# Optimization experiments

Measured on AMD Instinct MI355X. Metric: run time of the kernel, lower is better.

Reference implementation:

```python
import jax, jax.numpy as jnp
import numpy as np

D = 512       # d_model
H = 8         # n_heads
HD = D // H   # head_dim = 64
BS = 64       # block_size
B = 1
S = 8192
NB = S // BS  # 128 blocks
THRESH = 0.3


def setup_inputs() -> dict:
    key = jax.random.key(0)
    ks = jax.random.split(key, 6)
    sc = 0.02
    return {
        "x": jax.random.normal(ks[0], (B, S, D), jnp.float32),
        "w_qkv": (jax.random.normal(ks[1], (D, 3 * D)) * sc).astype(jnp.float32),
        "b_qkv": jnp.zeros((3 * D,), jnp.float32),
        "w_out": (jax.random.normal(ks[2], (D, D)) * sc).astype(jnp.float32),
        "b_out": jnp.zeros((D,), jnp.float32),
        "w_r1": (jax.random.normal(ks[3], (D, 128)) * sc).astype(jnp.float32),
        "b_r1": jnp.zeros((128,), jnp.float32),
        "w_r2": (jax.random.normal(ks[4], (128, 1)) * sc).astype(jnp.float32),
        "b_r2": jnp.full((1,), 0.5, jnp.float32),  # sigmoid(~0.5)>0.3 -> non-degenerate mask
    }


def reference(x, w_qkv, b_qkv, w_out, b_out, w_r1, b_r1, w_r2, b_r2):
    Bx, Sx, Dx = x.shape
    qkv = (x @ w_qkv + b_qkv).reshape(Bx, Sx, 3, H, HD)
    q = jnp.transpose(qkv[:, :, 0], (0, 2, 1, 3))  # [B,H,S,HD]
    k = jnp.transpose(qkv[:, :, 1], (0, 2, 1, 3))
    v = jnp.transpose(qkv[:, :, 2], (0, 2, 1, 3))

    # --- router: per-block importance from mean-pooled q block (d_model features) ---
    qb = q.reshape(Bx, H, NB, BS, HD)
    rep = jnp.transpose(qb.mean(axis=3), (0, 2, 1, 3)).reshape(Bx, NB, Dx)  # [B,NB,D]
    imp = jax.nn.sigmoid(jax.nn.relu(rep @ w_r1 + b_r1) @ w_r2 + b_r2)[..., 0]  # [B,NB]
    keep = (imp.mean(axis=0) >= THRESH).astype(x.dtype)  # [NB], shared across batch (torch uses batch-mean)

    kb = k.reshape(Bx, H, NB, BS, HD)
    vb = v.reshape(Bx, H, NB, BS, HD)
    tri = jnp.triu(jnp.ones((BS, BS), bool), 1)  # strict upper triangle within diagonal block
    jidx = jnp.arange(NB)
    scale = 1.0 / np.sqrt(HD)

    def step(carry, i):
        q_i = jax.lax.dynamic_slice_in_dim(q, i * BS, BS, axis=2)        # [B,H,BSq,HD]
        s = jnp.einsum('bhqd,bhjkd->bhqjk', q_i, kb) * scale             # [B,H,BSq,NB,BSk]
        causal = (jidx == i)[None, :, None] & tri[:, None, :]            # [BSq,NB,BSk]
        s = jnp.where(causal[None, None], -jnp.inf, s)
        p = jax.nn.softmax(s, axis=-1)                                   # softmax PER key-block (as in torch loop)
        wj = keep * keep[i]                                              # block pair gate [NB]
        o = jnp.einsum('bhqjk,j,bhjkd->bhqd', p, wj, vb)                 # sum of gated per-block contributions
        return carry, o

    _, outs = jax.lax.scan(step, None, jnp.arange(NB))                   # [NB,B,H,BSq,HD]
    attn = jnp.transpose(outs, (1, 2, 0, 3, 4)).reshape(Bx, H, Sx, HD)
    attn = jnp.transpose(attn, (0, 2, 1, 3)).reshape(Bx, Sx, Dx)
    return attn @ w_out + b_out
```

## Files before the change

### kernel.cpp

```cpp
#include <hip/hip_runtime.h>

typedef unsigned short u16;
typedef unsigned int u32;
typedef __attribute__((ext_vector_type(8))) short short8;
typedef __attribute__((ext_vector_type(4))) short short4v;
typedef __attribute__((ext_vector_type(4))) float f32x4;
typedef __attribute__((ext_vector_type(4))) float float4v;
typedef __attribute__((ext_vector_type(2))) u32 u32x2;
typedef __attribute__((ext_vector_type(4))) u32 u32x4;

#define S_LEN 8192
#define NHEAD 8
#define NBLK  128
#define SCALE_C 0.18033688011112042f

__device__ __forceinline__ u16 f2b(float f) {
    union { float f; unsigned u; } v; v.f = f;
    unsigned r = v.u + 0x7FFFu + ((v.u >> 16) & 1u);
    return (u16)(r >> 16);
}
__device__ __forceinline__ float b2f(u16 b) {
    union { float f; unsigned u; } v; v.u = ((unsigned)b) << 16; return v.f;
}
__device__ __forceinline__ u32 cvt_pk_bf16(float lo, float hi) {
    u32 r;
    asm("v_cvt_pk_bf16_f32 %0, %1, %2" : "=v"(r) : "v"(lo), "v"(hi));
    return r;
}
__device__ __forceinline__ void pl16swap(u32& a, u32& b) {
    u32x2 r = __builtin_amdgcn_permlane16_swap(a, b, false, false);
    a = r[0]; b = r[1];
}
__device__ __forceinline__ void pl32swap(u32& a, u32& b) {
    u32x2 r = __builtin_amdgcn_permlane32_swap(a, b, false, false);
    a = r[0]; b = r[1];
}
__device__ __forceinline__ int swz(int row, int colByte) {
    return row * 128 + (colByte ^ ((row & 7) << 4));
}
__device__ __forceinline__ void gload_lds(const void* g, void* l) {
    __builtin_amdgcn_global_load_lds(
        (const __attribute__((address_space(1))) void*)g,
        (__attribute__((address_space(3))) void*)l, 16, 0, 0);
}

__global__ __launch_bounds__(256) void cvt_x_kernel(const float* __restrict__ x, u16* __restrict__ xb) {
    int idx = blockIdx.x * 256 + threadIdx.x;
    float4v v = *((const float4v*)x + idx);
    short4v o;
    #pragma unroll
    for (int r = 0; r < 4; ++r) o[r] = (short)f2b(v[r]);
    *((short4v*)xb + idx) = o;
}

__global__ __launch_bounds__(256) void cvt_T_kernel(const float* __restrict__ w, u16* __restrict__ wt, int C) {
    int idx = blockIdx.x * 256 + threadIdx.x;
    int r = idx & 511, cc = idx >> 9;
    wt[idx] = f2b(w[(size_t)r * C + cc]);
}

__global__ __launch_bounds__(256) void sum4_kernel(const u16* __restrict__ a0, const u16* __restrict__ a1,
                                                   const u16* __restrict__ a2, const u16* __restrict__ a3,
                                                   int n, u16* __restrict__ outb) {
    int idx = blockIdx.x * 256 + threadIdx.x;
    short8 v0 = ((const short8*)a0)[idx];
    short8 v1 = ((const short8*)a1)[idx];
    float s[8];
    #pragma unroll
    for (int e = 0; e < 8; ++e) s[e] = b2f((u16)v0[e]) + b2f((u16)v1[e]);
    if (n == 4) {
        short8 v2 = ((const short8*)a2)[idx];
        short8 v3 = ((const short8*)a3)[idx];
        #pragma unroll
        for (int e = 0; e < 8; ++e) s[e] += b2f((u16)v2[e]) + b2f((u16)v3[e]);
    }
    short8 o;
    #pragma unroll
    for (int e = 0; e < 8; ++e) o[e] = (short)f2b(s[e]);
    ((short8*)outb)[idx] = o;
}

__device__ __forceinline__ void gemm128_core(const u16* __restrict__ A,
                                             const u16* __restrict__ Bt,
                                             int m0, int n0, char* As, char* Bs,
                                             f32x4 acc[4][4]) {
    const int tid = threadIdx.x;
    const int lane = tid & 63, wid = tid >> 6;
    const int q16 = lane >> 4, l16 = lane & 15;
    const int wm = wid >> 1, wn = wid & 1;
    #pragma unroll 1
    for (int kt = 0; kt < 8; ++kt) {
        const int k0 = kt * 64;
        __syncthreads();
        #pragma unroll
        for (int p = 0; p < 4; ++p) {
            int c = tid + p * 256;
            int row = c >> 3, colp = (c & 7) ^ (row & 7);
            gload_lds(A  + (size_t)(m0 + row) * 512 + k0 + colp * 8, As + (size_t)(wid * 64 + p * 256) * 16);
            gload_lds(Bt + (size_t)(n0 + row) * 512 + k0 + colp * 8, Bs + (size_t)(wid * 64 + p * 256) * 16);
        }
        __syncthreads();
        #pragma unroll
        for (int kk = 0; kk < 2; ++kk) {
            short8 a[4], b[4];
            #pragma unroll
            for (int t = 0; t < 4; ++t) {
                int arow = wm * 64 + t * 16 + l16;
                a[t] = *(const short8*)(As + swz(arow, kk * 64 + q16 * 16));
                int brow = wn * 64 + t * 16 + l16;
                b[t] = *(const short8*)(Bs + swz(brow, kk * 64 + q16 * 16));
            }
            #pragma unroll
            for (int mt = 0; mt < 4; ++mt)
                #pragma unroll
                for (int nt = 0; nt < 4; ++nt)
                    acc[mt][nt] = __builtin_amdgcn_mfma_f32_16x16x32_bf16(a[mt], b[nt], acc[mt][nt], 0, 0, 0);
        }
    }
}

__global__ __launch_bounds__(256) void qkv_gemm(const u16* __restrict__ xb, const u16* __restrict__ wqkvT,
                                                const float* __restrict__ bqkv,
                                                u16* __restrict__ qb, u16* __restrict__ kf, u16* __restrict__ vf) {
    __shared__ char smem[32768];
    f32x4 acc[4][4];
    #pragma unroll
    for (int a = 0; a < 4; ++a)
        #pragma unroll
        for (int b = 0; b < 4; ++b) acc[a][b] = (f32x4){0.f, 0.f, 0.f, 0.f};
    const int m0 = blockIdx.x * 128, n0 = blockIdx.y * 128;
    gemm128_core(xb, wqkvT, m0, n0, smem, smem + 16384, acc);

    const int lane = threadIdx.x & 63, wid = threadIdx.x >> 6;
    const int q16 = lane >> 4, l16 = lane & 15;
    const int wm = wid >> 1, wn = wid & 1;
    #pragma unroll
    for (int mt = 0; mt < 4; ++mt) {
        #pragma unroll
        for (int nt = 0; nt < 4; ++nt) {
            int n = n0 + wn * 64 + nt * 16 + l16;
            float bias = bqkv[n];
            int t = n >> 9, h = (n >> 6) & 7, d = n & 63;
            int sb = m0 + wm * 64 + mt * 16 + q16 * 4;
            f32x4 v = acc[mt][nt];
            if (t == 0) {
                #pragma unroll
                for (int r = 0; r < 4; ++r)
                    qb[(size_t)(h * S_LEN + sb + r) * 64 + d] = f2b((v[r] + bias) * SCALE_C);
            } else if (t == 1) {
                int j = sb >> 6, key = sb & 63;
                int n0k = key >> 4, c = d >> 5, q16k = (d >> 3) & 3, e = d & 7;
                int ub = (n0k * 2 + c) * 64 + q16k * 16 + (key & 15);
                u16* base = kf + (size_t)h * 524288 + (size_t)j * 4096 + e;
                #pragma unroll
                for (int r = 0; r < 4; ++r)
                    base[(ub + r) * 8] = f2b(v[r] + bias);
            } else {
                int j = sb >> 6, key = sb & 63;
                int dt = d >> 4, c = key >> 5, q16v = (key >> 3) & 3, e0 = key & 7;
                int u = (dt * 2 + c) * 64 + q16v * 16 + (d & 15);
                short4v pk;
                #pragma unroll
                for (int r = 0; r < 4; ++r) pk[r] = (short)f2b(v[r] + bias);
                *(short4v*)(vf + (size_t)h * 524288 + (size_t)j * 4096 + u * 8 + e0) = pk;
            }
        }
    }
}

__global__ __launch_bounds__(256) void out_gemm(const u16* __restrict__ a0, const u16* __restrict__ wotT,
                                                const float* __restrict__ bout, float* __restrict__ out) {
    __shared__ char smem[32768];
    f32x4 acc[4][4];
    #pragma unroll
    for (int a = 0; a < 4; ++a)
        #pragma unroll
        for (int b = 0; b < 4; ++b) acc[a][b] = (f32x4){0.f, 0.f, 0.f, 0.f};
    const int m0 = blockIdx.x * 128, n0 = blockIdx.y * 128;
    gemm128_core(a0, wotT, m0, n0, smem, smem + 16384, acc);

    const int lane = threadIdx.x & 63, wid = threadIdx.x >> 6;
    const int q16 = lane >> 4, l16 = lane & 15;
    const int wm = wid >> 1, wn = wid & 1;
    #pragma unroll
    for (int mt = 0; mt < 4; ++mt) {
        #pragma unroll
        for (int nt = 0; nt < 4; ++nt) {
            int n = n0 + wn * 64 + nt * 16 + l16;
            float bias = bout[n];
            int sb = m0 + wm * 64 + mt * 16 + q16 * 4;
            #pragma unroll
            for (int r = 0; r < 4; ++r)
                out[(size_t)(sb + r) * 512 + n] = acc[mt][nt][r] + bias;
        }
    }
}

__global__ __launch_bounds__(256) void router_kernel(const u16* __restrict__ qb,
                                                     const float* __restrict__ w_r1, const float* __restrict__ b_r1,
                                                     const float* __restrict__ w_r2, const float* __restrict__ b_r2,
                                                     float* __restrict__ keepf) {
    const int nb = blockIdx.x, tid = threadIdx.x;
    __shared__ float rep[512];
    __shared__ float h1[128];
    for (int dim = tid; dim < 512; dim += 256) {
        int h = dim >> 6, d = dim & 63;
        const u16* p = qb + (size_t)(h * S_LEN + nb * 64) * 64 + d;
        float s = 0.f;
        #pragma unroll 4
        for (int t = 0; t < 64; ++t) s += b2f(p[t * 64]);
        rep[dim] = s * (0.015625f / SCALE_C);
    }
    __syncthreads();
    if (tid < 128) {
        float a = b_r1[tid];
        for (int k = 0; k < 512; ++k) a += rep[k] * w_r1[k * 128 + tid];
        h1[tid] = fmaxf(a, 0.f);
    }
    __syncthreads();
    if (tid < 64) {
        float v = h1[tid] * w_r2[tid] + h1[tid + 64] * w_r2[tid + 64];
        #pragma unroll
        for (int off = 32; off; off >>= 1) v += __shfl_down(v, off);
        if (tid == 0) {
            float z = v + b_r2[0];
            keepf[nb] = (z >= -0.84729786f) ? 1.0f : 0.0f;
        }
    }
}

__global__ __launch_bounds__(256, 3) void attn_kernel(const u16* __restrict__ qb, const u16* __restrict__ kf,
                                                      const u16* __restrict__ vf, const float* __restrict__ keepf,
                                                      u16* __restrict__ a0, u16* __restrict__ a1,
                                                      u16* __restrict__ a2, u16* __restrict__ a3, int nj) {
    const int i = blockIdx.x, h = blockIdx.y, jh = blockIdx.z;
    const int j0 = jh * nj;
    u16* __restrict__ att = (jh == 0) ? a0 : (jh == 1) ? a1 : (jh == 2) ? a2 : a3;
    const int tid = threadIdx.x, lane = tid & 63, wid = tid >> 6;
    const int q16 = lane >> 4, l16 = lane & 15;
    __shared__ char smem[49152];

    short8 bq[2][2];
    #pragma unroll
    for (int qh = 0; qh < 2; ++qh) {
        const u16* qrow = qb + (size_t)(h * S_LEN + i * 128 + wid * 32 + qh * 16 + l16) * 64;
        bq[qh][0] = *(const short8*)(qrow + q16 * 8);
        bq[qh][1] = *(const short8*)(qrow + 32 + q16 * 8);
    }
    const int kq_s = __builtin_amdgcn_readfirstlane(i * 2 + (wid >> 1));
    const float keep_i = keepf[kq_s];
    const u32 kvbits = __builtin_bit_cast(u32, keepf[(j0 + lane) & 127]);
    const int qloc = (wid & 1) * 32 + l16;

    f32x4 o[2][4];
    #pragma unroll
    for (int qh = 0; qh < 2; ++qh)
        #pragma unroll
        for (int t = 0; t < 4; ++t) o[qh][t] = (f32x4){0.f, 0.f, 0.f, 0.f};

    const int lb = lane * 16;
    const int stoff = (wid * 128 + lane) * 8;
    const int ldw = wid * 2048;

    const u16* kst = kf + (size_t)h * 524288 + stoff + (size_t)j0 * 4096;
    const u16* vst = vf + (size_t)h * 524288 + stoff + (size_t)j0 * 4096;
    char *bA = smem, *bB = smem + 16384, *bC = smem + 32768;

    asm volatile("s_waitcnt vmcnt(0)" ::: "memory");

    gload_lds(kst,       bA + ldw);          gload_lds(kst + 512, bA + ldw + 1024);
    gload_lds(vst,       bA + 8192 + ldw);   gload_lds(vst + 512, bA + 8192 + ldw + 1024);
    kst += 4096; vst += 4096;
    gload_lds(kst,       bB + ldw);          gload_lds(kst + 512, bB + ldw + 1024);
    gload_lds(vst,       bB + 8192 + ldw);   gload_lds(vst + 512, bB + 8192 + ldw + 1024);
    kst += 4096; vst += 4096;

    for (int jj = 0; jj < nj; ++jj) {
        if (jj < nj - 1) asm volatile("s_waitcnt vmcnt(4)" ::: "memory");
        else             asm volatile("s_waitcnt vmcnt(0)" ::: "memory");
        __builtin_amdgcn_s_barrier();
        __builtin_amdgcn_sched_barrier(0);
        if (jj + 2 < nj) {
            gload_lds(kst,       bC + ldw);          gload_lds(kst + 512, bC + ldw + 1024);
            gload_lds(vst,       bC + 8192 + ldw);   gload_lds(vst + 512, bC + 8192 + ldw + 1024);
            kst += 4096; vst += 4096;
        }

        const int j = j0 + jj;
        const float kj = __builtin_bit_cast(float, (u32)__builtin_amdgcn_readlane((int)kvbits, jj));
        const float gj = keep_i * kj;
        char* Kc = bA;
        char* Vc = bA + 8192;

        f32x4 s4[2][4];
        __builtin_amdgcn_s_setprio(1);
        #pragma unroll
        for (int n0 = 0; n0 < 4; ++n0) {
            short8 ka0 = *(const short8*)(Kc + n0 * 2048 + lb);
            short8 ka1 = *(const short8*)(Kc + n0 * 2048 + 1024 + lb);
            #pragma unroll
            for (int qh = 0; qh < 2; ++qh) {
                f32x4 a = (f32x4){0.f, 0.f, 0.f, 0.f};
                a = __builtin_amdgcn_mfma_f32_16x16x32_bf16(ka0, bq[qh][0], a, 0, 0, 0);
                a = __builtin_amdgcn_mfma_f32_16x16x32_bf16(ka1, bq[qh][1], a, 0, 0, 0);
                s4[qh][n0] = a;
            }
        }
        __builtin_amdgcn_s_setprio(0);

        short8 pb[2][2];
        #pragma unroll
        for (int qh = 0; qh < 2; ++qh) {
            f32x4 p4[4];
            #pragma unroll
            for (int n0 = 0; n0 < 4; ++n0)
                #pragma unroll
                for (int r = 0; r < 4; ++r)
                    p4[n0][r] = __builtin_amdgcn_exp2f(s4[qh][n0][r]);
            if (j == kq_s) {
                const int qthis = qloc + qh * 16;
                #pragma unroll
                for (int n0 = 0; n0 < 4; ++n0)
                    #pragma unroll
                    for (int r = 0; r < 4; ++r)
                        if (n0 * 16 + q16 * 4 + r > qthis) p4[n0][r] = 0.f;
            }
            f32x4 sv = (p4[0] + p4[1]) + (p4[2] + p4[3]);
            float sum = (sv[0] + sv[1]) + (sv[2] + sv[3]);
            {
                u32 sa = __builtin_bit_cast(u32, sum), sb = sa;
                pl16swap(sa, sb);
                sum = __builtin_bit_cast(float, sa) + __builtin_bit_cast(float, sb);
                u32 sc = __builtin_bit_cast(u32, sum), sd = sc;
                pl32swap(sc, sd);
                sum = __builtin_bit_cast(float, sc) + __builtin_bit_cast(float, sd);
            }
            const float rinv = gj * __builtin_amdgcn_rcpf(sum);
            u32 dw[4][2];
            #pragma unroll
            for (int n0 = 0; n0 < 4; ++n0) {
                f32x4 t = p4[n0] * rinv;
                dw[n0][0] = cvt_pk_bf16(t[0], t[1]);
                dw[n0][1] = cvt_pk_bf16(t[2], t[3]);
            }
            #pragma unroll
            for (int kk = 0; kk < 2; ++kk) {
                u32 c0 = dw[2 * kk][0], d0 = dw[2 * kk + 1][0];
                pl32swap(c0, d0);
                pl16swap(c0, d0);
                u32 c1 = dw[2 * kk][1], d1 = dw[2 * kk + 1][1];
                pl32swap(c1, d1);
                pl16swap(c1, d1);
                u32x4 wv;
                wv[0] = c0; wv[1] = c1; wv[2] = d0; wv[3] = d1;
                pb[qh][kk] = __builtin_bit_cast(short8, wv);
            }
        }

        __builtin_amdgcn_s_setprio(1);
        #pragma unroll
        for (int dt = 0; dt < 4; ++dt) {
            short8 va0 = *(const short8*)(Vc + dt * 2048 + lb);
            short8 va1 = *(const short8*)(Vc + dt * 2048 + 1024 + lb);
            #pragma unroll
            for (int qh = 0; qh < 2; ++qh) {
                o[qh][dt] = __builtin_amdgcn_mfma_f32_16x16x32_bf16(va0, pb[qh][0], o[qh][dt], 0, 0, 0);
                o[qh][dt] = __builtin_amdgcn_mfma_f32_16x16x32_bf16(va1, pb[qh][1], o[qh][dt], 0, 0, 0);
            }
        }
        __builtin_amdgcn_s_setprio(0);

        char* tmp = bA; bA = bB; bB = bC; bC = tmp;
    }

    #pragma unroll
    for (int qh = 0; qh < 2; ++qh) {
        u16* obase = att + (size_t)(i * 128 + wid * 32 + qh * 16 + l16) * 512 + h * 64 + q16 * 4;
        #pragma unroll
        for (int dt = 0; dt < 4; ++dt) {
            u32x2 st;
            st[0] = cvt_pk_bf16(o[qh][dt][0], o[qh][dt][1]);
            st[1] = cvt_pk_bf16(o[qh][dt][2], o[qh][dt][3]);
            *(u32x2*)(obase + dt * 16) = st;
        }
    }
}

static const size_t OFF_WQKVT = 0;
static const size_t OFF_WOTT  = (size_t)2u << 20;
static const size_t OFF_KEEP  = ((size_t)2u << 20) + (512u << 10);
static const size_t OFF_QB    = (size_t)3u << 20;
static const size_t OFF_KF    = (size_t)11u << 20;
static const size_t OFF_VF    = (size_t)19u << 20;
static const size_t OFF_XB    = (size_t)27u << 20;
static const size_t OFF_P0    = (size_t)35u << 20;
static const size_t OFF_P1    = (size_t)43u << 20;
static const size_t OFF_P2    = (size_t)51u << 20;

extern "C" void kernel_launch(void* const* d_in, const int* in_sizes, int n_in,
                              void* d_out, int out_size, void* d_ws, size_t ws_size,
                              hipStream_t stream) {
    const float* x     = (const float*)d_in[0];
    const float* w_qkv = (const float*)d_in[1];
    const float* b_qkv = (const float*)d_in[2];
    const float* w_out = (const float*)d_in[3];
    const float* b_out = (const float*)d_in[4];
    const float* w_r1  = (const float*)d_in[5];
    const float* b_r1  = (const float*)d_in[6];
    const float* w_r2  = (const float*)d_in[7];
    const float* b_r2  = (const float*)d_in[8];
    float* out = (float*)d_out;
    char* ws = (char*)d_ws;
    u16* wqkvT  = (u16*)(ws + OFF_WQKVT);
    u16* wotT   = (u16*)(ws + OFF_WOTT);
    float* keepf = (float*)(ws + OFF_KEEP);
    u16* qb     = (u16*)(ws + OFF_QB);
    u16* kf     = (u16*)(ws + OFF_KF);
    u16* vf     = (u16*)(ws + OFF_VF);
    u16* xb     = (u16*)(ws + OFF_XB);
    u16* attnb  = (u16*)(ws + OFF_QB);

    const bool big = ws_size >= ((size_t)59u << 20) + 4096;
    const int njh = big ? 4 : 2;
    const int nj  = NBLK / njh;
    u16* a0 = (u16*)(ws + OFF_P0);
    u16* a1 = big ? (u16*)(ws + OFF_P1) : (u16*)(ws + OFF_XB);
    u16* a2 = big ? (u16*)(ws + OFF_P2) : a0;
    u16* a3 = big ? (u16*)(ws + OFF_XB) : a0;

    cvt_x_kernel<<<4096, 256, 0, stream>>>(x, xb);
    cvt_T_kernel<<<3072, 256, 0, stream>>>(w_qkv, wqkvT, 1536);
    cvt_T_kernel<<<1024, 256, 0, stream>>>(w_out, wotT, 512);
    qkv_gemm<<<dim3(64, 12), 256, 0, stream>>>(xb, wqkvT, b_qkv, qb, kf, vf);
    router_kernel<<<128, 256, 0, stream>>>(qb, w_r1, b_r1, w_r2, b_r2, keepf);
    attn_kernel<<<dim3(64, 8, njh), 256, 0, stream>>>(qb, kf, vf, keepf, a0, a1, a2, a3, nj);
    sum4_kernel<<<2048, 256, 0, stream>>>(a0, a1, a2, a3, njh, attnb);
    out_gemm<<<dim3(64, 4), 256, 0, stream>>>(attnb, wotT, b_out, out);
}
```

Measured before the change: 245.4 us.

## Software-pipeline QK^T of the next key block with softmax and PV of the current

Restructures the attention inner loop into a two-stage software pipeline. The QK^T MFMAs for block jj+1 are issued before the exp/normalise/PV work for block jj, using two ping-ponged score register sets. The aim is to overlap matrix work with the transcendental and permute-heavy softmax. In exchange, each iteration now waits for all outstanding global-to-LDS loads (vmcnt(0)) rather than leaving one stage in flight, and register pressure rises. The unrolled-by-two loop with its fixed tail appears to assume an even block count of at least two.

```diff
diff --git a/kernel.cpp b/kernel.cpp
--- a/kernel.cpp
+++ b/kernel.cpp
@@ -268,31 +268,12 @@
 
     asm volatile("s_waitcnt vmcnt(0)" ::: "memory");
 
-    gload_lds(kst,       bA + ldw);          gload_lds(kst + 512, bA + ldw + 1024);
-    gload_lds(vst,       bA + 8192 + ldw);   gload_lds(vst + 512, bA + 8192 + ldw + 1024);
-    kst += 4096; vst += 4096;
-    gload_lds(kst,       bB + ldw);          gload_lds(kst + 512, bB + ldw + 1024);
-    gload_lds(vst,       bB + 8192 + ldw);   gload_lds(vst + 512, bB + 8192 + ldw + 1024);
-    kst += 4096; vst += 4096;
-
-    for (int jj = 0; jj < nj; ++jj) {
-        if (jj < nj - 1) asm volatile("s_waitcnt vmcnt(4)" ::: "memory");
-        else             asm volatile("s_waitcnt vmcnt(0)" ::: "memory");
-        __builtin_amdgcn_s_barrier();
-        __builtin_amdgcn_sched_barrier(0);
-        if (jj + 2 < nj) {
-            gload_lds(kst,       bC + ldw);          gload_lds(kst + 512, bC + ldw + 1024);
-            gload_lds(vst,       bC + 8192 + ldw);   gload_lds(vst + 512, bC + 8192 + ldw + 1024);
-            kst += 4096; vst += 4096;
-        }
-
-        const int j = j0 + jj;
-        const float kj = __builtin_bit_cast(float, (u32)__builtin_amdgcn_readlane((int)kvbits, jj));
-        const float gj = keep_i * kj;
-        char* Kc = bA;
-        char* Vc = bA + 8192;
-
-        f32x4 s4[2][4];
+    auto STAGE = [&](char* dst) {
+        gload_lds(kst,       dst + ldw);          gload_lds(kst + 512, dst + ldw + 1024);
+        gload_lds(vst,       dst + 8192 + ldw);   gload_lds(vst + 512, dst + 8192 + ldw + 1024);
+        kst += 4096; vst += 4096;
+    };
+    auto QK = [&](const char* Kc, f32x4 (&s)[2][4]) {
         __builtin_amdgcn_s_setprio(1);
         #pragma unroll
         for (int n0 = 0; n0 < 4; ++n0) {
@@ -303,11 +284,15 @@
                 f32x4 a = (f32x4){0.f, 0.f, 0.f, 0.f};
                 a = __builtin_amdgcn_mfma_f32_16x16x32_bf16(ka0, bq[qh][0], a, 0, 0, 0);
                 a = __builtin_amdgcn_mfma_f32_16x16x32_bf16(ka1, bq[qh][1], a, 0, 0, 0);
-                s4[qh][n0] = a;
+                s[qh][n0] = a;
             }
         }
         __builtin_amdgcn_s_setprio(0);
-
+    };
+    auto SMPV = [&](int jjl, const f32x4 (&s)[2][4], const char* Vc) {
+        const float kj = __builtin_bit_cast(float, (u32)__builtin_amdgcn_readlane((int)kvbits, jjl));
+        const float gj = keep_i * kj;
+        const int j = j0 + jjl;
         short8 pb[2][2];
         #pragma unroll
         for (int qh = 0; qh < 2; ++qh) {
@@ -316,7 +301,7 @@
             for (int n0 = 0; n0 < 4; ++n0)
                 #pragma unroll
                 for (int r = 0; r < 4; ++r)
-                    p4[n0][r] = __builtin_amdgcn_exp2f(s4[qh][n0][r]);
+                    p4[n0][r] = __builtin_amdgcn_exp2f(s[qh][n0][r]);
             if (j == kq_s) {
                 const int qthis = qloc + qh * 16;
                 #pragma unroll
@@ -356,7 +341,6 @@
                 pb[qh][kk] = __builtin_bit_cast(short8, wv);
             }
         }
-
         __builtin_amdgcn_s_setprio(1);
         #pragma unroll
         for (int dt = 0; dt < 4; ++dt) {
@@ -369,9 +353,40 @@
             }
         }
         __builtin_amdgcn_s_setprio(0);
-
-        char* tmp = bA; bA = bB; bB = bC; bC = tmp;
-    }
+    };
+    auto WAITBAR = [&]() {
+        asm volatile("s_waitcnt vmcnt(0)" ::: "memory");
+        __builtin_amdgcn_s_barrier();
+        __builtin_amdgcn_sched_barrier(0);
+    };
+    auto ROT = [&]() { char* t = bA; bA = bB; bB = bC; bC = t; };
+
+    STAGE(bA);
+    STAGE(bB);
+    asm volatile("s_waitcnt vmcnt(4)" ::: "memory");
+    __builtin_amdgcn_s_barrier();
+
+    f32x4 sA[2][4], sB[2][4];
+    QK(bA, sA);
+
+    for (int jj = 0; jj + 3 < nj; jj += 2) {
+        WAITBAR();
+        STAGE(bC);
+        QK(bB, sB);
+        SMPV(jj, sA, bA + 8192);
+        ROT();
+        WAITBAR();
+        STAGE(bC);
+        QK(bB, sA);
+        SMPV(jj + 1, sB, bA + 8192);
+        ROT();
+    }
+    WAITBAR();
+    QK(bB, sB);
+    SMPV(nj - 2, sA, bA + 8192);
+    ROT();
+    WAITBAR();
+    SMPV(nj - 1, sB, bA + 8192);
 
     #pragma unroll
     for (int qh = 0; qh < 2; ++qh) {
```

New measurement: 240.3 us. 2.1% less time.
